# Performance work log

Hardware: AMD Instinct MI355X
Metric: run time of the kernel (lower is better)

The kernel has to match this reference:

```python
import jax, jax.numpy as jnp
import numpy as np

N, M, C, T, H, W = 32, 20, 512, 4, 7, 7  # batch, max_others, channels, t, h, w
L = 4  # temp_pos_len
STD = 0.01


def setup_inputs() -> dict:
    key = jax.random.key(0)
    ks = jax.random.split(key, 12)
    return {
        "person": jax.random.normal(ks[0], (N, C, T, H, W), jnp.float32),
        "others": jax.random.normal(ks[1], (N, M, C, T, H, W), jnp.float32),
        "Wq": jax.random.normal(ks[2], (C, C), jnp.float32) * STD,
        "bq": jax.random.normal(ks[3], (C,), jnp.float32) * STD,
        "Wk": jax.random.normal(ks[4], (C, C), jnp.float32) * STD,
        "bk": jax.random.normal(ks[5], (C,), jnp.float32) * STD,
        "Wv": jax.random.normal(ks[6], (C, C), jnp.float32) * STD,
        "bv": jax.random.normal(ks[7], (C,), jnp.float32) * STD,
        "Wo": jax.random.normal(ks[8], (C, C), jnp.float32) * STD,
        "bo": jax.random.normal(ks[9], (C,), jnp.float32) * STD,
        "pos_k": jax.random.normal(ks[10], (L, C), jnp.float32) * 0.02,
        "pos_v": jax.random.normal(ks[11], (L, C), jnp.float32) * 0.02,
    }


def reference(person, others, Wq, bq, Wk, bk, Wv, bv, Wo, bo, pos_k, pos_v):
    n, c, t, h, w = person.shape
    _, m, _, to, ho, wo = others.shape
    scale = c ** (-0.5)

    # 1x1x1 conv projections == channel matmuls
    q = jnp.einsum('oc,ncthw->nothw', Wq, person) + bq[None, :, None, None, None]
    k = jnp.einsum('oc,nmcthw->nmothw', Wk, others) + bk[None, None, :, None, None, None]
    v = jnp.einsum('oc,nmcthw->nmothw', Wv, others) + bv[None, None, :, None, None, None]

    # additive temporal positional bias on K/V: others split into L temporal groups
    Lp = pos_k.shape[0]
    P = m // Lp  # max_person_per_sec
    k = (k.reshape(n, Lp, P, c, to, ho, wo)
         + pos_k[None, :, None, :, None, None, None]).reshape(n, m, c, to, ho, wo)
    v = (v.reshape(n, Lp, P, c, to, ho, wo)
         + pos_v[None, :, None, :, None, None, None]).reshape(n, m, c, to, ho, wo)

    S = t * h * w          # query length
    K = m * to * ho * wo   # key length
    qf = q.reshape(n, c, S).transpose(0, 2, 1)                              # [n,S,c]
    kf = k.reshape(n, m, c, to * ho * wo).transpose(0, 1, 3, 2).reshape(n, K, c)
    vf = v.reshape(n, m, c, to * ho * wo).transpose(0, 1, 3, 2).reshape(n, K, c)

    attn = jax.nn.softmax(jnp.einsum('nsc,nkc->nsk', qf, kf) * scale, axis=-1)
    o = jnp.einsum('nsk,nkc->nsc', attn, vf)                                # [n,S,c]
    o = o.transpose(0, 2, 1).reshape(n, c, t, h, w)

    # LayerNorm over [c,t,h,w] per sample, no affine
    mu = jnp.mean(o, axis=(1, 2, 3, 4), keepdims=True)
    var = jnp.var(o, axis=(1, 2, 3, 4), keepdims=True)
    o = (o - mu) * jax.lax.rsqrt(var + 1e-5)

    o = jax.nn.relu(o)
    o = jnp.einsum('oc,ncthw->nothw', Wo, o) + bo[None, :, None, None, None]
    return o + person  # shortcut is identity (dim_person == dim_out)
```

## Files before the change

### kernel.cpp

```cpp
#include <hip/hip_runtime.h>
#include <hip/hip_bf16.h>

#define N_B 32
#define M_O 20
#define C_C 512
#define S_S 196
#define S_P 208
#define K_K 3920
#define K_P 4096
#define SCALEF 0.044194173824159216f

typedef short s4v __attribute__((ext_vector_type(4)));
typedef short s8v __attribute__((ext_vector_type(8)));
typedef float f4v __attribute__((ext_vector_type(4)));

__device__ __forceinline__ f4v mfma16(s8v a, s8v b, f4v c){
  return __builtin_amdgcn_mfma_f32_16x16x32_bf16(a, b, c, 0, 0, 0);
}
__device__ __forceinline__ unsigned short f2b(float x){
  __hip_bfloat16 h = __float2bfloat16(x);
  return *reinterpret_cast<unsigned short*>(&h);
}
__device__ __forceinline__ float b2f(short u){
  unsigned int v = ((unsigned int)(unsigned short)u) << 16;
  return __uint_as_float(v);
}

#define GLOAD16(g, l) __builtin_amdgcn_global_load_lds( \
    (const __attribute__((address_space(1))) unsigned int*)(g), \
    (__attribute__((address_space(3))) unsigned int*)(l), 16, 0, 0)

__global__ void k_sentinel(float* out, float v){ out[threadIdx.x] = v; }

__global__ void k_cvt(const float* __restrict__ w0, const float* __restrict__ w1,
                      const float* __restrict__ w2, const float* __restrict__ w3,
                      unsigned short* __restrict__ out){
  int i = blockIdx.x*256 + threadIdx.x;
  int m = i >> 16;
  int r = i & 65535;
  const float* s = (m==0)?w0:((m==1)?w1:((m==2)?w2:w3));
  f4v v = ((const f4v*)s)[r];
  s4v o = { (short)f2b(v[0]), (short)f2b(v[1]), (short)f2b(v[2]), (short)f2b(v[3]) };
  ((s4v*)out)[i] = o;
}

__global__ __launch_bounds__(256) void k_tr(const float* __restrict__ X,
                                            unsigned short* __restrict__ Xt){
  const int cc = blockIdx.x * 64;
  const int slab = blockIdx.y;
  const int tid = threadIdx.x;
  __shared__ unsigned short A[196][72];
  const int row = tid >> 2;
  const int j   = tid & 3;
  const float* src = X + (size_t)slab*(C_C*S_S) + (size_t)(cc+row)*S_S;
  for (int p = j; p < 49; p += 4){
    f4v v = *(const f4v*)(src + p*4);
    int s = p*4;
    A[s+0][row] = f2b(v[0]);
    A[s+1][row] = f2b(v[1]);
    A[s+2][row] = f2b(v[2]);
    A[s+3][row] = f2b(v[3]);
  }
  __syncthreads();
  unsigned short* dst = Xt + (size_t)slab*(S_S*C_C) + cc;
  for (int v = tid; v < S_S*8; v += 256){
    int s = v >> 3, c8 = v & 7;
    *(s8v*)(dst + (size_t)s*C_C + c8*8) = *(const s8v*)&A[s][c8*8];
  }
}

template<bool HASV>
__global__ __launch_bounds__(256, 2) void k_projgemm(
    const unsigned short* __restrict__ Xt,
    const unsigned short* __restrict__ W1, const float* __restrict__ b1, const float* __restrict__ pos1,
    const unsigned short* __restrict__ W2, const float* __restrict__ b2, const float* __restrict__ pos2,
    unsigned short* __restrict__ outK, unsigned short* __restrict__ outVT)
{
  const int id = blockIdx.x;
  const int work = HASV ? ((id & 7)*980 + (id >> 3)) : id;
  const int ct    = HASV ? (work & 3) : (work & 1);
  const int rtile = HASV ? (work >> 2) : (work >> 1);
  const int r0 = rtile*64;
  const int cb = ct * (HASV ? 128 : 256);
  const int tid = threadIdx.x, wid = tid>>6, lane = tid&63;
  const int lr = lane&15, lq = lane>>4;
  const int mat = wid >> 1, chalf = (wid & 1)*64;
  const bool isV = HASV && (mat == 1);

  const unsigned short* WB = HASV ? W2 : W1;
  const int cbB = HASV ? cb : cb + 128;

  __shared__ unsigned short SA[2][2048];
  __shared__ unsigned short SB[2][8192];

  f4v acc[4][4];
  #pragma unroll
  for (int i=0;i<4;i++)
    #pragma unroll
    for (int j=0;j<4;j++) acc[i][j]=(f4v){0,0,0,0};

  const int rsub = lane >> 2;
  const int csub = ((lane & 3) ^ ((rsub>>1)&3)) * 8;

  auto STAGE = [&](int buf, int c0){
    const unsigned short* ga = Xt + (size_t)(r0 + wid*16 + rsub)*C_C + c0 + csub;
    GLOAD16(ga, &SA[buf][(wid*16)*32]);
    #pragma unroll
    for (int j=0;j<4;j++){
      const int br = j*64 + wid*16 + rsub;
      const unsigned short* gw = (j<2)
        ? W1 + (size_t)(cb  + br      )*C_C + c0 + csub
        : WB + (size_t)(cbB + br - 128)*C_C + c0 + csub;
      GLOAD16(gw, &SB[buf][(j*64 + wid*16)*32]);
    }
  };

  STAGE(0, 0);

  const int bbase = mat*128 + chalf;
  const int rchunk = (lq ^ ((lr>>1)&3)) * 8;
  for (int it = 0; it < 16; ++it){
    const int buf = it & 1;
    if (it < 15){
      STAGE(buf^1, (it+1)*32);
      asm volatile("s_waitcnt vmcnt(5)" ::: "memory");
    } else {
      asm volatile("s_waitcnt vmcnt(0)" ::: "memory");
    }
    __builtin_amdgcn_s_barrier();
    s8v af[4], bf[4];
    #pragma unroll
    for (int i=0;i<4;i++)
      af[i] = *(const s8v*)&SA[buf][(i*16 + lr)*32 + rchunk];
    #pragma unroll
    for (int i=0;i<4;i++)
      bf[i] = *(const s8v*)&SB[buf][(bbase + i*16 + lr)*32 + rchunk];
    if (!isV){
      #pragma unroll
      for (int ot=0;ot<4;ot++)
        #pragma unroll
        for (int rt=0;rt<4;rt++)
          acc[rt][ot] = mfma16(af[rt], bf[ot], acc[rt][ot]);
    } else {
      #pragma unroll
      for (int ot=0;ot<4;ot++)
        #pragma unroll
        for (int rt=0;rt<4;rt++)
          acc[ot][rt] = mfma16(bf[ot], af[rt], acc[ot][rt]);
    }
    __builtin_amdgcn_s_barrier();
  }

  const int cout = HASV ? (cb + chalf) : (cb + mat*128 + chalf);
  if (!isV){
    #pragma unroll
    for (int ot=0;ot<4;ot++){
      const int o = cout + ot*16 + lr;
      const float bb = b1[o];
      #pragma unroll
      for (int rt=0;rt<4;rt++){
        #pragma unroll
        for (int rr=0;rr<4;rr++){
          const int r = r0 + rt*16 + lq*4 + rr;
          float bias = bb;
          if (HASV) bias += pos1[((r % K_K)/980)*C_C + o];
          outK[(size_t)r*C_C + o] = f2b(acc[rt][ot][rr] + bias);
        }
      }
    }
  } else {
    #pragma unroll
    for (int ot=0;ot<4;ot++){
      #pragma unroll
      for (int rr=0;rr<4;rr++){
        const int o = cout + ot*16 + lq*4 + rr;
        const float bb = b2[o];
        #pragma unroll
        for (int rt=0;rt<4;rt++){
          const int r = r0 + rt*16 + lr;
          const int n = r / K_K;
          const int rn = r - n*K_K;
          const float bias = bb + pos2[(rn/980)*C_C + o];
          outVT[(size_t)n*C_C*K_P + (size_t)o*K_P + rn] = f2b(acc[ot][rt][rr] + bias);
        }
      }
    }
  }
}

template<int MODE>
__global__ __launch_bounds__(512, 2) void k_gemm(
    const unsigned short* __restrict__ A, const unsigned short* __restrict__ B,
    unsigned short* __restrict__ out16, float* __restrict__ out32)
{
  constexpr int LDA = (MODE==3)?4096:512;
  constexpr int LDB = (MODE==3)?4096:512;
  constexpr int NIT = (MODE==3)?64:16;

  const int tid = threadIdx.x, wid = tid>>6, lane = tid&63;
  const int lr = lane&15, lq = lane>>4;
  const int wr = wid>>2, wc = wid&3;

  int rtile, ctsel, nslab = 0, ks = 0;
  if constexpr (MODE==2){
    int x = blockIdx.x & 7, idx = blockIdx.x >> 3;
    int w = x*128 + idx; nslab = w >> 5; int sub = w & 31;
    ctsel = sub & 15; rtile = sub >> 4;
  } else {
    int x = blockIdx.x & 7, idx = blockIdx.x >> 3;
    int w = x*32 + idx; nslab = w >> 3; int sub = w & 7;
    ks = sub >> 2; rtile = (sub>>1)&1; ctsel = sub & 1;
  }
  const int r0 = rtile*128;
  int koff = 0;
  const unsigned short* Aslab; const unsigned short* Bslab;
  if constexpr (MODE==2){
    Aslab = A + (size_t)nslab*S_S*C_C;
    Bslab = B + (size_t)nslab*K_K*C_C + ctsel*256*512;
  } else {
    Aslab = A + (size_t)nslab*S_P*K_P;
    Bslab = B + (size_t)nslab*C_C*K_P + (size_t)ctsel*256*4096;
    koff = ks*2048;
  }

  __shared__ unsigned short SA[2][4096];
  __shared__ unsigned short SB[2][8192];

  f4v acc[4][4];
  #pragma unroll
  for (int i=0;i<4;i++)
    #pragma unroll
    for (int j=0;j<4;j++) acc[i][j]=(f4v){0,0,0,0};

  const int rsub = lane >> 2;
  const int csub = ((lane & 3) ^ ((rsub>>1)&3)) * 8;

  auto STAGE = [&](int buf, int c0){
    GLOAD16(Aslab + (size_t)(r0 + wid*16 + rsub)*LDA + c0 + csub,
            &SA[buf][(wid*16)*32]);
    GLOAD16(Bslab + (size_t)(wid*16 + rsub)*LDB + c0 + csub,
            &SB[buf][(wid*16)*32]);
    GLOAD16(Bslab + (size_t)(128 + wid*16 + rsub)*LDB + c0 + csub,
            &SB[buf][(128 + wid*16)*32]);
  };

  STAGE(0, koff);

  const int rchunk = (lq ^ ((lr>>1)&3)) * 8;
  for (int it = 0; it < NIT; ++it){
    const int buf = it & 1;
    if (it + 1 < NIT){
      STAGE(buf^1, koff + (it+1)*32);
      asm volatile("s_waitcnt vmcnt(3)" ::: "memory");
    } else {
      asm volatile("s_waitcnt vmcnt(0)" ::: "memory");
    }
    __builtin_amdgcn_s_barrier();
    s8v af[4], bf[4];
    #pragma unroll
    for (int i=0;i<4;i++)
      af[i] = *(const s8v*)&SA[buf][(wr*64 + i*16 + lr)*32 + rchunk];
    #pragma unroll
    for (int j=0;j<4;j++)
      bf[j] = *(const s8v*)&SB[buf][(wc*64 + j*16 + lr)*32 + rchunk];
    #pragma unroll
    for (int ot=0;ot<4;ot++)
      #pragma unroll
      for (int rt=0;rt<4;rt++)
        acc[rt][ot] = mfma16(af[rt], bf[ot], acc[rt][ot]);
    __builtin_amdgcn_s_barrier();
  }

  if constexpr (MODE==2){
    #pragma unroll
    for (int ot=0;ot<4;ot++){
      const int kcol = ctsel*256 + wc*64 + ot*16 + lr;
      #pragma unroll
      for (int rt=0;rt<4;rt++){
        #pragma unroll
        for (int rr=0;rr<4;rr++){
          const int s = r0 + wr*64 + rt*16 + lq*4 + rr;
          if (s < S_P){
            unsigned short v = (kcol < K_K) ? f2b(acc[rt][ot][rr]) : (unsigned short)0;
            out16[((size_t)nslab*S_P + s)*K_P + kcol] = v;
          }
        }
      }
    }
  } else {
    float* op = out32 + (size_t)ks*(N_B*S_P*C_C);
    #pragma unroll
    for (int ot=0;ot<4;ot++){
      const int c = ctsel*256 + wc*64 + ot*16 + lr;
      #pragma unroll
      for (int rt=0;rt<4;rt++){
        #pragma unroll
        for (int rr=0;rr<4;rr++){
          const int s = r0 + wr*64 + rt*16 + lq*4 + rr;
          if (s < S_P)
            op[((size_t)nslab*S_P + s)*C_C + c] = acc[rt][ot][rr];
        }
      }
    }
  }
}

__global__ __launch_bounds__(256) void k_softmax(unsigned short* __restrict__ Sb){
  const int row = blockIdx.x;
  const int n = row / S_S, s = row - n*S_S;
  unsigned short* p = Sb + ((size_t)n*S_P + s)*K_P;
  const int tid = threadIdx.x;
  const bool valid = tid < 245;
  float x[16];
  if (valid){
    s8v v0 = *(const s8v*)(p + tid*16);
    s8v v1 = *(const s8v*)(p + tid*16 + 8);
    #pragma unroll
    for (int i=0;i<8;i++){ x[i]=b2f(v0[i]); x[8+i]=b2f(v1[i]); }
  } else {
    #pragma unroll
    for (int i=0;i<16;i++) x[i] = -1e30f;
  }
  float mx = x[0];
  #pragma unroll
  for (int i=1;i<16;i++) mx = fmaxf(mx, x[i]);
  #pragma unroll
  for (int d=32;d>=1;d>>=1) mx = fmaxf(mx, __shfl_xor(mx, d));
  __shared__ float red1[4], red2[4];
  if ((tid&63)==0) red1[tid>>6]=mx;
  __syncthreads();
  mx = fmaxf(fmaxf(red1[0],red1[1]),fmaxf(red1[2],red1[3]));
  float sum = 0.f;
  #pragma unroll
  for (int i=0;i<16;i++){ x[i]=__expf((x[i]-mx)*SCALEF); sum+=x[i]; }
  #pragma unroll
  for (int d=32;d>=1;d>>=1) sum += __shfl_xor(sum, d);
  if ((tid&63)==0) red2[tid>>6]=sum;
  __syncthreads();
  sum = red2[0]+red2[1]+red2[2]+red2[3];
  float inv = 1.f/sum;
  unsigned short o16[16];
  #pragma unroll
  for (int i=0;i<16;i++) o16[i] = f2b(x[i]*inv);
  if (valid){
    *(s8v*)(p + tid*16) = *(const s8v*)o16;
    *(s8v*)(p + tid*16 + 8) = *(const s8v*)(o16+8);
  }
}

__global__ void k_lnpart(const float* __restrict__ O0, const float* __restrict__ O1,
                         float* __restrict__ sums){
  const int part = blockIdx.x, n = blockIdx.y;
  const int tid = threadIdx.x;
  const size_t base = ((size_t)n*S_P + part*49)*C_C;
  float ls=0.f, ls2=0.f;
  for (int i = tid; i < 49*C_C/4; i += 256){
    f4v a = ((const f4v*)(O0+base))[i];
    f4v b = ((const f4v*)(O1+base))[i];
    #pragma unroll
    for (int j=0;j<4;j++){ float v = a[j]+b[j]; ls += v; ls2 += v*v; }
  }
  #pragma unroll
  for (int d=32;d>=1;d>>=1){ ls += __shfl_xor(ls,d); ls2 += __shfl_xor(ls2,d); }
  __shared__ float r1[4], r2[4];
  if ((tid&63)==0){ r1[tid>>6]=ls; r2[tid>>6]=ls2; }
  __syncthreads();
  if (tid==0){
    atomicAdd(&sums[n*2],   r1[0]+r1[1]+r1[2]+r1[3]);
    atomicAdd(&sums[n*2+1], r2[0]+r2[1]+r2[2]+r2[3]);
  }
}

__global__ void k_norm(const float* __restrict__ O0, const float* __restrict__ O1,
                       const float* __restrict__ sums, unsigned short* __restrict__ ob){
  size_t g = (size_t)blockIdx.x*256 + threadIdx.x;
  int n = (int)(g / (S_P*C_C/8));
  int rem = (int)(g - (size_t)n*(S_P*C_C/8));
  int s = rem / (C_C/8);
  const float inv = 1.f/((float)S_S*C_C);
  float mu = sums[n*2]*inv;
  float var = sums[n*2+1]*inv - mu*mu;
  float rq = rsqrtf(var + 1e-5f);
  const f4v* s0 = (const f4v*)(O0 + g*8);
  const f4v* s1 = (const f4v*)(O1 + g*8);
  f4v a0 = s0[0], a1 = s0[1], b0 = s1[0], b1 = s1[1];
  unsigned short o16[8];
  if (s < S_S){
    #pragma unroll
    for (int i=0;i<4;i++){ float y=(a0[i]+b0[i]-mu)*rq; o16[i]=f2b(fmaxf(y,0.f)); }
    #pragma unroll
    for (int i=0;i<4;i++){ float y=(a1[i]+b1[i]-mu)*rq; o16[4+i]=f2b(fmaxf(y,0.f)); }
  } else {
    #pragma unroll
    for (int i=0;i<8;i++) o16[i]=0;
  }
  *(s8v*)(ob + g*8) = *(const s8v*)o16;
}

__global__ __launch_bounds__(256) void k_final(const unsigned short* __restrict__ ob,
    const unsigned short* __restrict__ Wo, const float* __restrict__ bo,
    const float* __restrict__ person, float* __restrict__ out)
{
  const int ocb = blockIdx.x, n = blockIdx.y;
  const int tid=threadIdx.x, wid=tid>>6, lane=tid&63, lr=lane&15, lq=lane>>4;
  const int ocb0 = ocb*64 + wid*16;
  const unsigned short* obp = ob + (size_t)n*S_P*C_C;
  f4v acc[13];
  #pragma unroll
  for (int i=0;i<13;i++) acc[i]=(f4v){0,0,0,0};
  for (int c0=0;c0<C_C;c0+=32){
    s8v af = *(const s8v*)(Wo + (size_t)(ocb0+lr)*C_C + c0 + lq*8);
    #pragma unroll
    for (int ct=0;ct<13;ct++){
      s8v bfv = *(const s8v*)(obp + (size_t)(ct*16+lr)*C_C + c0 + lq*8);
      acc[ct]=mfma16(af,bfv,acc[ct]);
    }
  }
  #pragma unroll
  for (int ct=0;ct<13;ct++){
    #pragma unroll
    for (int r=0;r<4;r++){
      int oc = ocb0 + lq*4 + r;
      int s = ct*16 + lr;
      if (s < S_S){
        size_t idx = ((size_t)n*C_C + oc)*S_S + s;
        out[idx] = acc[ct][r] + bo[oc] + person[idx];
      }
    }
  }
}

extern "C" void kernel_launch(void* const* d_in, const int* in_sizes, int n_in,
                              void* d_out, int out_size, void* d_ws, size_t ws_size,
                              hipStream_t stream)
{
  (void)in_sizes; (void)n_in; (void)out_size;
  const float* person = (const float*)d_in[0];
  const float* others = (const float*)d_in[1];
  const float* Wq = (const float*)d_in[2];
  const float* bq = (const float*)d_in[3];
  const float* Wk = (const float*)d_in[4];
  const float* bk = (const float*)d_in[5];
  const float* Wv = (const float*)d_in[6];
  const float* bv = (const float*)d_in[7];
  const float* Wo = (const float*)d_in[8];
  const float* bo = (const float*)d_in[9];
  const float* pos_k = (const float*)d_in[10];
  const float* pos_v = (const float*)d_in[11];
  float* out = (float*)d_out;

  char* ws = (char*)d_ws;
  size_t off = 0;
  auto alloc = [&](size_t bytes)->char*{
    char* p = ws + off; off += (bytes + 255) & ~(size_t)255; return p;
  };
  unsigned short* Wb  = (unsigned short*)alloc(4ull*C_C*C_C*2);
  unsigned short* Xt  = (unsigned short*)alloc(((size_t)N_B*M_O*S_S + 16)*C_C*2);
  unsigned short* Qt  = (unsigned short*)alloc(((size_t)N_B*S_S + 16)*C_C*2);
  unsigned short* qb  = (unsigned short*)alloc(((size_t)N_B*S_S + 64)*C_C*2);
  unsigned short* kfb = (unsigned short*)alloc(((size_t)N_B*K_K + 256)*C_C*2);
  unsigned short* vtb = (unsigned short*)alloc((size_t)N_B*C_C*K_P*2);
  float* sums         = (float*)alloc(2*N_B*sizeof(float));

  size_t aoff = 0;
  auto alias = [&](size_t bytes)->char*{
    char* p = (char*)Xt + aoff; aoff += (bytes + 255) & ~(size_t)255; return p;
  };
  unsigned short* Sbuf = (unsigned short*)alias(((size_t)N_B*S_P + 64)*K_P*2);
  float* Obuf          = (float*)alias(2ull*N_B*S_P*C_C*4);
  unsigned short* obb  = (unsigned short*)alias((size_t)N_B*S_P*C_C*2);

  if (off > ws_size) {
    k_sentinel<<<1,256,0,stream>>>(out, (float)(ws_size>>20));
    return;
  }

  unsigned short* Wq_b = Wb;
  unsigned short* Wk_b = Wb + 262144;
  unsigned short* Wv_b = Wb + 2*262144;
  unsigned short* Wo_b = Wb + 3*262144;
  float* O1 = Obuf + (size_t)N_B*S_P*C_C;

  hipMemsetAsync(sums, 0, 2*N_B*sizeof(float), stream);
  k_cvt<<<1024,256,0,stream>>>(Wq,Wk,Wv,Wo,Wb);
  k_tr<<<dim3(8,N_B*M_O),256,0,stream>>>(others, Xt);
  k_tr<<<dim3(8,N_B),256,0,stream>>>(person, Qt);
  k_projgemm<true ><<<7840,256,0,stream>>>(Xt,
      Wk_b, bk, pos_k, Wv_b, bv, pos_v, kfb, vtb);
  k_projgemm<false><<<196,256,0,stream>>>(Qt,
      Wq_b, bq, nullptr, nullptr, nullptr, nullptr, qb, nullptr);
  k_gemm<2><<<1024,512,0,stream>>>(qb, kfb, Sbuf, nullptr);
  k_softmax<<<N_B*S_S,256,0,stream>>>(Sbuf);
  k_gemm<3><<<256,512,0,stream>>>(Sbuf, vtb, nullptr, Obuf);
  k_lnpart<<<dim3(4,N_B),256,0,stream>>>(Obuf, O1, sums);
  k_norm<<<1664,256,0,stream>>>(Obuf, O1, sums, obb);
  k_final<<<dim3(8,N_B),256,0,stream>>>(obb, Wo_b, bo, person, out);
}
```

Baseline: 590.2 us.

## Fuse softmax exp into score GEMM and defer normalization to PV epilogue

The standalone softmax kernel is removed. The score GEMM now applies exp(score*scale) in its epilogue, stores unnormalized bf16 probabilities and atomically accumulates per-row sums. The PV GEMM divides its outputs by the row sum. This drops a full read and write pass over the score matrix and one launch. It also drops the max subtraction, which risks overflow for large scores, and the PV kernel is retiled to 256 threads with a 128x128 tile and 512 blocks.

```diff
diff --git a/kernel.cpp b/kernel.cpp
--- a/kernel.cpp
+++ b/kernel.cpp
@@ -188,40 +188,21 @@
   }
 }
 
-template<int MODE>
-__global__ __launch_bounds__(512, 2) void k_gemm(
+__global__ __launch_bounds__(512, 2) void k_scores(
     const unsigned short* __restrict__ A, const unsigned short* __restrict__ B,
-    unsigned short* __restrict__ out16, float* __restrict__ out32)
+    unsigned short* __restrict__ out16, float* __restrict__ rowsum)
 {
-  constexpr int LDA = (MODE==3)?4096:512;
-  constexpr int LDB = (MODE==3)?4096:512;
-  constexpr int NIT = (MODE==3)?64:16;
-
   const int tid = threadIdx.x, wid = tid>>6, lane = tid&63;
   const int lr = lane&15, lq = lane>>4;
   const int wr = wid>>2, wc = wid&3;
 
-  int rtile, ctsel, nslab = 0, ks = 0;
-  if constexpr (MODE==2){
-    int x = blockIdx.x & 7, idx = blockIdx.x >> 3;
-    int w = x*128 + idx; nslab = w >> 5; int sub = w & 31;
-    ctsel = sub & 15; rtile = sub >> 4;
-  } else {
-    int x = blockIdx.x & 7, idx = blockIdx.x >> 3;
-    int w = x*32 + idx; nslab = w >> 3; int sub = w & 7;
-    ks = sub >> 2; rtile = (sub>>1)&1; ctsel = sub & 1;
-  }
+  int x = blockIdx.x & 7, idx = blockIdx.x >> 3;
+  int w = x*128 + idx;
+  const int nslab = w >> 5; int sub = w & 31;
+  const int ctsel = sub & 15, rtile = sub >> 4;
   const int r0 = rtile*128;
-  int koff = 0;
-  const unsigned short* Aslab; const unsigned short* Bslab;
-  if constexpr (MODE==2){
-    Aslab = A + (size_t)nslab*S_S*C_C;
-    Bslab = B + (size_t)nslab*K_K*C_C + ctsel*256*512;
-  } else {
-    Aslab = A + (size_t)nslab*S_P*K_P;
-    Bslab = B + (size_t)nslab*C_C*K_P + (size_t)ctsel*256*4096;
-    koff = ks*2048;
-  }
+  const unsigned short* Aslab = A + (size_t)nslab*S_S*C_C;
+  const unsigned short* Bslab = B + (size_t)nslab*K_K*C_C + (size_t)ctsel*256*512;
 
   __shared__ unsigned short SA[2][4096];
   __shared__ unsigned short SB[2][8192];
@@ -236,21 +217,21 @@
   const int csub = ((lane & 3) ^ ((rsub>>1)&3)) * 8;
 
   auto STAGE = [&](int buf, int c0){
-    GLOAD16(Aslab + (size_t)(r0 + wid*16 + rsub)*LDA + c0 + csub,
+    GLOAD16(Aslab + (size_t)(r0 + wid*16 + rsub)*512 + c0 + csub,
             &SA[buf][(wid*16)*32]);
-    GLOAD16(Bslab + (size_t)(wid*16 + rsub)*LDB + c0 + csub,
+    GLOAD16(Bslab + (size_t)(wid*16 + rsub)*512 + c0 + csub,
             &SB[buf][(wid*16)*32]);
-    GLOAD16(Bslab + (size_t)(128 + wid*16 + rsub)*LDB + c0 + csub,
+    GLOAD16(Bslab + (size_t)(128 + wid*16 + rsub)*512 + c0 + csub,
             &SB[buf][(128 + wid*16)*32]);
   };
 
-  STAGE(0, koff);
+  STAGE(0, 0);
 
   const int rchunk = (lq ^ ((lr>>1)&3)) * 8;
-  for (int it = 0; it < NIT; ++it){
+  for (int it = 0; it < 16; ++it){
     const int buf = it & 1;
-    if (it + 1 < NIT){
-      STAGE(buf^1, koff + (it+1)*32);
+    if (it < 15){
+      STAGE(buf^1, (it+1)*32);
       asm volatile("s_waitcnt vmcnt(3)" ::: "memory");
     } else {
       asm volatile("s_waitcnt vmcnt(0)" ::: "memory");
@@ -271,80 +252,133 @@
     __builtin_amdgcn_s_barrier();
   }
 
-  if constexpr (MODE==2){
-    #pragma unroll
-    for (int ot=0;ot<4;ot++){
-      const int kcol = ctsel*256 + wc*64 + ot*16 + lr;
-      #pragma unroll
-      for (int rt=0;rt<4;rt++){
-        #pragma unroll
-        for (int rr=0;rr<4;rr++){
-          const int s = r0 + wr*64 + rt*16 + lq*4 + rr;
-          if (s < S_P){
-            unsigned short v = (kcol < K_K) ? f2b(acc[rt][ot][rr]) : (unsigned short)0;
-            out16[((size_t)nslab*S_P + s)*K_P + kcol] = v;
-          }
-        }
+  float psum[4][4];
+  #pragma unroll
+  for (int rt=0;rt<4;rt++)
+    #pragma unroll
+    for (int rr=0;rr<4;rr++) psum[rt][rr] = 0.f;
+
+  #pragma unroll
+  for (int ot=0;ot<4;ot++){
+    const int kcol = ctsel*256 + wc*64 + ot*16 + lr;
+    #pragma unroll
+    for (int rt=0;rt<4;rt++){
+      #pragma unroll
+      for (int rr=0;rr<4;rr++){
+        const int s = r0 + wr*64 + rt*16 + lq*4 + rr;
+        float e = (kcol < K_K) ? __expf(acc[rt][ot][rr]*SCALEF) : 0.f;
+        psum[rt][rr] += e;
+        if (s < S_P)
+          out16[((size_t)nslab*S_P + s)*K_P + kcol] = f2b(e);
       }
     }
-  } else {
-    float* op = out32 + (size_t)ks*(N_B*S_P*C_C);
-    #pragma unroll
-    for (int ot=0;ot<4;ot++){
-      const int c = ctsel*256 + wc*64 + ot*16 + lr;
-      #pragma unroll
-      for (int rt=0;rt<4;rt++){
-        #pragma unroll
-        for (int rr=0;rr<4;rr++){
-          const int s = r0 + wr*64 + rt*16 + lq*4 + rr;
-          if (s < S_P)
-            op[((size_t)nslab*S_P + s)*C_C + c] = acc[rt][ot][rr];
-        }
+  }
+  #pragma unroll
+  for (int rt=0;rt<4;rt++){
+    #pragma unroll
+    for (int rr=0;rr<4;rr++){
+      float v = psum[rt][rr];
+      v += __shfl_xor(v, 1);
+      v += __shfl_xor(v, 2);
+      v += __shfl_xor(v, 4);
+      v += __shfl_xor(v, 8);
+      if (lr == 0){
+        const int s = r0 + wr*64 + rt*16 + lq*4 + rr;
+        if (s < S_P) atomicAdd(&rowsum[nslab*S_P + s], v);
       }
     }
   }
 }
 
-__global__ __launch_bounds__(256) void k_softmax(unsigned short* __restrict__ Sb){
-  const int row = blockIdx.x;
-  const int n = row / S_S, s = row - n*S_S;
-  unsigned short* p = Sb + ((size_t)n*S_P + s)*K_P;
-  const int tid = threadIdx.x;
-  const bool valid = tid < 245;
-  float x[16];
-  if (valid){
-    s8v v0 = *(const s8v*)(p + tid*16);
-    s8v v1 = *(const s8v*)(p + tid*16 + 8);
-    #pragma unroll
-    for (int i=0;i<8;i++){ x[i]=b2f(v0[i]); x[8+i]=b2f(v1[i]); }
-  } else {
-    #pragma unroll
-    for (int i=0;i<16;i++) x[i] = -1e30f;
-  }
-  float mx = x[0];
-  #pragma unroll
-  for (int i=1;i<16;i++) mx = fmaxf(mx, x[i]);
-  #pragma unroll
-  for (int d=32;d>=1;d>>=1) mx = fmaxf(mx, __shfl_xor(mx, d));
-  __shared__ float red1[4], red2[4];
-  if ((tid&63)==0) red1[tid>>6]=mx;
-  __syncthreads();
-  mx = fmaxf(fmaxf(red1[0],red1[1]),fmaxf(red1[2],red1[3]));
-  float sum = 0.f;
-  #pragma unroll
-  for (int i=0;i<16;i++){ x[i]=__expf((x[i]-mx)*SCALEF); sum+=x[i]; }
-  #pragma unroll
-  for (int d=32;d>=1;d>>=1) sum += __shfl_xor(sum, d);
-  if ((tid&63)==0) red2[tid>>6]=sum;
-  __syncthreads();
-  sum = red2[0]+red2[1]+red2[2]+red2[3];
-  float inv = 1.f/sum;
-  unsigned short o16[16];
-  #pragma unroll
-  for (int i=0;i<16;i++) o16[i] = f2b(x[i]*inv);
-  if (valid){
-    *(s8v*)(p + tid*16) = *(const s8v*)o16;
-    *(s8v*)(p + tid*16 + 8) = *(const s8v*)(o16+8);
+__global__ __launch_bounds__(256, 2) void k_pv(
+    const unsigned short* __restrict__ A, const unsigned short* __restrict__ B,
+    const float* __restrict__ rowsum, float* __restrict__ out32)
+{
+  const int tid = threadIdx.x, wid = tid>>6, lane = tid&63;
+  const int lr = lane&15, lq = lane>>4;
+  const int wr = wid>>1, wc = wid&1;
+
+  int x = blockIdx.x & 7, idx = blockIdx.x >> 3;
+  int w = x*64 + idx;
+  const int nslab = w >> 4; int sub = w & 15;
+  const int ks = sub >> 3, rtile = (sub>>2)&1, ctsel = sub & 3;
+  const int r0 = rtile*128;
+  const int koff = ks*2048;
+  const unsigned short* Aslab = A + (size_t)nslab*S_P*K_P;
+  const unsigned short* Bslab = B + (size_t)nslab*C_C*K_P + (size_t)ctsel*128*K_P;
+
+  __shared__ unsigned short SA[2][4096];
+  __shared__ unsigned short SB[2][4096];
+
+  f4v acc[4][4];
+  #pragma unroll
+  for (int i=0;i<4;i++)
+    #pragma unroll
+    for (int j=0;j<4;j++) acc[i][j]=(f4v){0,0,0,0};
+
+  const int rsub = lane >> 2;
+  const int csub = ((lane & 3) ^ ((rsub>>1)&3)) * 8;
+
+  auto STAGE = [&](int buf, int c0){
+    GLOAD16(Aslab + (size_t)(r0 + wid*16 + rsub)*K_P + c0 + csub,
+            &SA[buf][(wid*16)*32]);
+    GLOAD16(Aslab + (size_t)(r0 + 64 + wid*16 + rsub)*K_P + c0 + csub,
+            &SA[buf][(64 + wid*16)*32]);
+    GLOAD16(Bslab + (size_t)(wid*16 + rsub)*K_P + c0 + csub,
+            &SB[buf][(wid*16)*32]);
+    GLOAD16(Bslab + (size_t)(64 + wid*16 + rsub)*K_P + c0 + csub,
+            &SB[buf][(64 + wid*16)*32]);
+  };
+
+  STAGE(0, koff);
+
+  const int rchunk = (lq ^ ((lr>>1)&3)) * 8;
+  for (int it = 0; it < 64; ++it){
+    const int buf = it & 1;
+    if (it < 63){
+      STAGE(buf^1, koff + (it+1)*32);
+      asm volatile("s_waitcnt vmcnt(4)" ::: "memory");
+    } else {
+      asm volatile("s_waitcnt vmcnt(0)" ::: "memory");
+    }
+    __builtin_amdgcn_s_barrier();
+    s8v af[4], bf[4];
+    #pragma unroll
+    for (int i=0;i<4;i++)
+      af[i] = *(const s8v*)&SA[buf][(wr*64 + i*16 + lr)*32 + rchunk];
+    #pragma unroll
+    for (int j=0;j<4;j++)
+      bf[j] = *(const s8v*)&SB[buf][(wc*64 + j*16 + lr)*32 + rchunk];
+    #pragma unroll
+    for (int ot=0;ot<4;ot++)
+      #pragma unroll
+      for (int rt=0;rt<4;rt++)
+        acc[rt][ot] = mfma16(af[rt], bf[ot], acc[rt][ot]);
+    __builtin_amdgcn_s_barrier();
+  }
+
+  float invs[4][4];
+  #pragma unroll
+  for (int rt=0;rt<4;rt++){
+    #pragma unroll
+    for (int rr=0;rr<4;rr++){
+      const int s = r0 + wr*64 + rt*16 + lq*4 + rr;
+      invs[rt][rr] = (s < S_P) ? 1.f/rowsum[(size_t)nslab*S_P + s] : 0.f;
+    }
+  }
+  float* op = out32 + (size_t)ks*(N_B*S_P*C_C);
+  #pragma unroll
+  for (int ot=0;ot<4;ot++){
+    const int c = ctsel*128 + wc*64 + ot*16 + lr;
+    #pragma unroll
+    for (int rt=0;rt<4;rt++){
+      #pragma unroll
+      for (int rr=0;rr<4;rr++){
+        const int s = r0 + wr*64 + rt*16 + lq*4 + rr;
+        if (s < S_P)
+          op[((size_t)nslab*S_P + s)*C_C + c] = acc[rt][ot][rr]*invs[rt][rr];
+      }
+    }
   }
 }
 
@@ -461,6 +495,7 @@
   unsigned short* kfb = (unsigned short*)alloc(((size_t)N_B*K_K + 256)*C_C*2);
   unsigned short* vtb = (unsigned short*)alloc((size_t)N_B*C_C*K_P*2);
   float* sums         = (float*)alloc(2*N_B*sizeof(float));
+  float* rowsum       = (float*)alloc((size_t)N_B*S_P*sizeof(float));
 
   size_t aoff = 0;
   auto alias = [&](size_t bytes)->char*{
@@ -482,6 +517,7 @@
   float* O1 = Obuf + (size_t)N_B*S_P*C_C;
 
   hipMemsetAsync(sums, 0, 2*N_B*sizeof(float), stream);
+  hipMemsetAsync(rowsum, 0, (size_t)N_B*S_P*sizeof(float), stream);
   k_cvt<<<1024,256,0,stream>>>(Wq,Wk,Wv,Wo,Wb);
   k_tr<<<dim3(8,N_B*M_O),256,0,stream>>>(others, Xt);
   k_tr<<<dim3(8,N_B),256,0,stream>>>(person, Qt);
@@ -489,9 +525,8 @@
       Wk_b, bk, pos_k, Wv_b, bv, pos_v, kfb, vtb);
   k_projgemm<false><<<196,256,0,stream>>>(Qt,
       Wq_b, bq, nullptr, nullptr, nullptr, nullptr, qb, nullptr);
-  k_gemm<2><<<1024,512,0,stream>>>(qb, kfb, Sbuf, nullptr);
-  k_softmax<<<N_B*S_S,256,0,stream>>>(Sbuf);
-  k_gemm<3><<<256,512,0,stream>>>(Sbuf, vtb, nullptr, Obuf);
+  k_scores<<<1024,512,0,stream>>>(qb, kfb, Sbuf, rowsum);
+  k_pv<<<512,256,0,stream>>>(Sbuf, vtb, rowsum, Obuf);
   k_lnpart<<<dim3(4,N_B),256,0,stream>>>(Obuf, O1, sums);
   k_norm<<<1664,256,0,stream>>>(Obuf, O1, sums, obb);
   k_final<<<dim3(8,N_B),256,0,stream>>>(obb, Wo_b, bo, person, out);
```

After: 581.6 us. No clear change (-1.5%).
